# Performance work log

Measured on AMD Instinct MI355X. Metric: run time of the kernel, lower is better.

## Reference

```python
import jax, jax.numpy as jnp
import numpy as np

N, F_IN, D, R, E = 50000, 128, 96, 2, 800000


def setup_inputs() -> dict:
    key = jax.random.key(0)
    ks = jax.random.split(key, 8)
    sc = lambda k, shape: jax.random.normal(k, shape, jnp.float32) * 0.05
    return {
        "x": jax.random.normal(ks[0], (N, F_IN), jnp.float32),
        "edge_index": jax.random.randint(ks[1], (2, E), 0, N),
        "edge_attr": jax.random.uniform(ks[2], (E, R), dtype=jnp.float32),
        # nn.Linear(F_IN, D)
        "Wf": sc(ks[3], (D, F_IN)),
        "bf": jnp.zeros((D,), jnp.float32),
        # RGCNConv: per-relation weights, root weight, bias
        "W": sc(ks[4], (R, D, D)),
        "root": sc(ks[5], (D, D)),
        "bias": jnp.zeros((D,), jnp.float32),
    }


def _rgcn_conv(h, src, dst, etype, W, root, bias):
    # PyG RGCNConv (no bases/blocks, aggr='mean'):
    #   out = x @ root + bias + sum_r mean_{edges of type r}(x[src]) @ W[r]
    msg = h[src]  # [E, D] gather
    out = h @ root + bias
    for r in range(R):
        w = (etype == r).astype(h.dtype)[:, None]  # [E, 1] relation mask
        s = jax.ops.segment_sum(msg * w, dst, num_segments=N)   # [N, D] scatter-add
        cnt = jax.ops.segment_sum(w, dst, num_segments=N)       # [N, 1]
        agg = s / jnp.maximum(cnt, 1.0)                          # mean, safe for deg 0
        out = out + agg @ W[r]
    return out


def reference(x, edge_index, edge_attr, Wf, bf, W, root, bias):
    src, dst = edge_index[0], edge_index[1]
    etype = jnp.argmax(edge_attr, axis=1)  # [E]
    h = jax.nn.relu(x @ Wf.T + bf)
    for _ in range(3):
        h = jax.nn.relu(_rgcn_conv(h, src, dst, etype, W, root, bias))
    return h
```

## Files before the change

kernel.cpp:

```cpp
#include <hip/hip_runtime.h>

#define DN 96
#define FIN 128

typedef unsigned int uint_t;
typedef unsigned short ushort_t;

typedef __attribute__((ext_vector_type(8))) short short8v;
typedef __attribute__((ext_vector_type(4))) float f32x4;

#define MFMA16 __builtin_amdgcn_mfma_f32_16x16x32_bf16

struct __align__(4) U3 { uint_t x, y, z; };

__device__ __forceinline__ ushort_t f2bf(float f) {
    uint_t u = __float_as_uint(f);
    uint_t r = (u + 0x7FFFu + ((u >> 16) & 1u)) >> 16;
    return (ushort_t)r;
}
__device__ __forceinline__ float bf2f(ushort_t h) { return __uint_as_float(((uint_t)h) << 16); }
__device__ __forceinline__ float bf_lo(uint_t u) { return __uint_as_float(u << 16); }
__device__ __forceinline__ float bf_hi(uint_t u) { return __uint_as_float(u & 0xFFFF0000u); }

__device__ __forceinline__ U3 ldrow(const uint_t* __restrict__ g, int idx, int j) {
    return *(const U3*)(g + (size_t)idx * 48 + 3 * j);
}
__device__ __forceinline__ void acc6(float* s, U3 v) {
    s[0] += bf_lo(v.x); s[1] += bf_hi(v.x);
    s[2] += bf_lo(v.y); s[3] += bf_hi(v.y);
    s[4] += bf_lo(v.z); s[5] += bf_hi(v.z);
}


__global__ __launch_bounds__(256) void prep_kernel(
    const int* __restrict__ ei, const float* __restrict__ ea,
    uint_t* __restrict__ kdx, ushort_t* __restrict__ kdy,
    const float* __restrict__ root, const float* __restrict__ W, const float* __restrict__ Wf,
    ushort_t* __restrict__ Bph, ushort_t* __restrict__ Bpl,
    ushort_t* __restrict__ Wfh, ushort_t* __restrict__ Wfl,
    ushort_t* g0A, ushort_t* g1A, ushort_t* g0B, ushort_t* g1B,
    int E, int N, int KD_BLKS)
{
    int bid = blockIdx.x;
    int t = threadIdx.x;
    if (bid < KD_BLKS) {
        int e = bid * 256 + t;
        if (e < E) {
            int src = ei[e];
            int dst = ei[E + e];
            float2 a = *(const float2*)(ea + 2 * e);
            int r = (a.y > a.x) ? 1 : 0;
            kdx[e] = (uint_t)dst | ((uint_t)r << 16);
            kdy[e] = (ushort_t)src;
        }
    } else if (bid < KD_BLKS + 78) {
        if (t >= 64) return;
        int l = t;
        int fid = bid - KD_BLKS;
        if (fid < 54) {
            int ct = fid / 3, ks = fid % 3;
            int mat = ct / 6, cw = ct % 6;
            const float* M = (mat == 0) ? root : (W + (size_t)(mat - 1) * DN * DN);
            int k0 = 32 * ks + (l >> 4) * 8;
            int col = 16 * cw + (l & 15);
#pragma unroll
            for (int j = 0; j < 8; j++) {
                float v = M[(size_t)(k0 + j) * DN + col];
                ushort_t h = f2bf(v);
                size_t idx = ((size_t)fid * 64 + l) * 8 + j;
                Bph[idx] = h;
                Bpl[idx] = f2bf(v - bf2f(h));
            }
        } else {
            int f2 = fid - 54;
            int ct = f2 >> 2, ks = f2 & 3;
            int k0 = 32 * ks + (l >> 4) * 8;
            int col = 16 * ct + (l & 15);
#pragma unroll
            for (int j = 0; j < 8; j++) {
                float v = Wf[(size_t)col * FIN + k0 + j];
                ushort_t h = f2bf(v);
                size_t idx = ((size_t)f2 * 64 + l) * 8 + j;
                Wfh[idx] = h;
                Wfl[idx] = f2bf(v - bf2f(h));
            }
        }
    } else {
        int pair = bid - (KD_BLKS + 78);
        ushort_t* ga = pair ? g0B : g0A;
        ushort_t* gb = pair ? g1B : g1A;
        if (t < 96) ga[(size_t)N * DN + t] = 0;
        else if (t < 192) gb[(size_t)N * DN + (t - 96)] = 0;
    }
}


__global__ __launch_bounds__(256) void hist_part(const uint_t* __restrict__ kdx,
                                                 int* __restrict__ cnt, int E, int N, int PS) {
    int p = blockIdx.x & 7;
    int c = blockIdx.x >> 3;
    int base = c * 2048 + threadIdx.x;
#pragma unroll
    for (int i = 0; i < 8; i++) {
        int e = base + i * 256;
        if (e < E) {
            uint_t v = kdx[e];
            int dst = v & 0xFFFF;
            if (dst / PS == p) {
                int r = (v >> 16) & 1;
                atomicAdd(&cnt[r * N + dst], 1);
            }
        }
    }
}

__global__ void offsets_kernel(const int* __restrict__ cnt, int* __restrict__ total,
                               int* __restrict__ rowstart, int* __restrict__ fillptr,
                               int nbins) {
    __shared__ int sd[256];
    __shared__ int sbase;
    int t = threadIdx.x;
    int b = blockIdx.x * 256 + t;
    int v = (b < nbins) ? cnt[b] : 0;
    sd[t] = v;
    __syncthreads();
    for (int off = 1; off < 256; off <<= 1) {
        int add = (t >= off) ? sd[t - off] : 0;
        __syncthreads();
        sd[t] += add;
        __syncthreads();
    }
    if (t == 255) sbase = atomicAdd(total, sd[255]);
    __syncthreads();
    if (b < nbins) {
        int s = sbase + sd[t] - v;
        rowstart[b] = s;
        fillptr[b] = s;
    }
}


__global__ __launch_bounds__(256) void fill_part(const uint_t* __restrict__ kdx,
                            const ushort_t* __restrict__ kdy,
                            int* __restrict__ fillptr, ushort_t* __restrict__ srcs,
                            int E, int N, int PS) {
    int p = blockIdx.x & 7;
    int c = blockIdx.x >> 3;
    int base = c * 2048 + threadIdx.x;
#pragma unroll
    for (int i = 0; i < 8; i++) {
        int e = base + i * 256;
        if (e < E) {
            uint_t v = kdx[e];
            int dst = v & 0xFFFF;
            if (dst / PS == p) {
                int r = (v >> 16) & 1;
                int pos = atomicAdd(&fillptr[r * N + dst], 1);
                srcs[pos] = kdy[e];
            }
        }
    }
}


__device__ __forceinline__ void cvt8(float4 x, float4 y, short8v& hi, short8v& lo) {
    union { short8v v; ushort_t u[8]; } H, L;
    float f[8] = {x.x, x.y, x.z, x.w, y.x, y.y, y.z, y.w};
#pragma unroll
    for (int j = 0; j < 8; j++) {
        ushort_t h = f2bf(f[j]);
        H.u[j] = h;
        L.u[j] = f2bf(f[j] - bf2f(h));
    }
    hi = H.v; lo = L.v;
}


__global__ __launch_bounds__(256) void lin_gemm(
    const float* __restrict__ xin,
    const ushort_t* __restrict__ WfH, const ushort_t* __restrict__ WfL,
    const ushort_t* __restrict__ Bph, const ushort_t* __restrict__ Bpl,
    const float* __restrict__ bfv, const float* __restrict__ bias,
    float* __restrict__ hrootOut, ushort_t* __restrict__ g0Out, ushort_t* __restrict__ g1Out,
    int N)
{
    __shared__ float sout[4][16][100];
    int t = threadIdx.x;
    int l = t & 63;
    int w = t >> 6;

    int slab = blockIdx.x * 64 + w * 16;
    int row = slab + (l & 15);
    if (row >= N) row = N - 1;
    const float* xrow = xin + (size_t)row * FIN + ((l >> 4) * 8);
    short8v ah4[4], al4[4];
#pragma unroll
    for (int ks = 0; ks < 4; ks++) {
        float4 xa = *(const float4*)(xrow + 32 * ks);
        float4 xb = *(const float4*)(xrow + 32 * ks + 4);
        cvt8(xa, xb, ah4[ks], al4[ks]);
    }
#pragma unroll
    for (int ct = 0; ct < 6; ct++) {
        f32x4 hh = {0.f,0.f,0.f,0.f}, hl_ = {0.f,0.f,0.f,0.f}, lh = {0.f,0.f,0.f,0.f};
#pragma unroll
        for (int ks = 0; ks < 4; ks++) {
            size_t base = ((size_t)(ct * 4 + ks) * 64 + l) * 8;
            short8v bh = *(const short8v*)(WfH + base);
            short8v bl = *(const short8v*)(WfL + base);
            hh  = MFMA16(ah4[ks], bh, hh, 0, 0, 0);
            hl_ = MFMA16(ah4[ks], bl, hl_, 0, 0, 0);
            lh  = MFMA16(al4[ks], bh, lh, 0, 0, 0);
        }
        f32x4 acc = hh + hl_ + lh;
        int col = ct * 16 + (l & 15);
        float bv = bfv[col];
        int lr0 = (l >> 4) * 4;
#pragma unroll
        for (int r = 0; r < 4; r++) {
            float v = acc[r] + bv;
            sout[w][lr0 + r][col] = v > 0.f ? v : 0.f;
        }
    }
    __syncthreads();

    const float* srow = &sout[w][l & 15][0];
    int mbase = blockIdx.x * 64 + w * 16 + ((l >> 4) << 2);
    int k0 = (l >> 4) * 8;
    short8v ah[3], al[3];
#pragma unroll
    for (int ks = 0; ks < 3; ks++) {
        float4 xa = *(const float4*)(srow + k0 + 32 * ks);
        float4 xb = *(const float4*)(srow + k0 + 32 * ks + 4);
        cvt8(xa, xb, ah[ks], al[ks]);
    }
    for (int ct = 0; ct < 18; ct++) {
        f32x4 hh = {0.f,0.f,0.f,0.f}, hl_ = {0.f,0.f,0.f,0.f}, lh = {0.f,0.f,0.f,0.f};
#pragma unroll
        for (int ks = 0; ks < 3; ks++) {
            size_t base = ((size_t)(ct * 3 + ks) * 64 + l) * 8;
            short8v bh = *(const short8v*)(Bph + base);
            short8v bl = *(const short8v*)(Bpl + base);
            hh  = MFMA16(ah[ks], bh, hh, 0, 0, 0);
            hl_ = MFMA16(ah[ks], bl, hl_, 0, 0, 0);
            lh  = MFMA16(al[ks], bh, lh, 0, 0, 0);
        }
        f32x4 acc = hh + hl_ + lh;
        int mat = ct / 6;
        int col = (ct % 6) * 16 + (l & 15);
        if (mat == 0) {
            float bv = bias[col];
#pragma unroll
            for (int r = 0; r < 4; r++) {
                int m = mbase + r;
                if (m < N) hrootOut[(size_t)m * DN + col] = acc[r] + bv;
            }
        } else {
            ushort_t* g = (mat == 1) ? g0Out : g1Out;
#pragma unroll
            for (int r = 0; r < 4; r++) {
                int m = mbase + r;
                if (m < N) g[(size_t)m * DN + col] = f2bf(acc[r]);
            }
        }
    }
}


template <int GEMM>
__global__ __launch_bounds__(256) void layer_kernel(
    const float* __restrict__ hrootIn,
    const uint_t* __restrict__ g0In, const uint_t* __restrict__ g1In,
    const int* __restrict__ rowstart, const int* __restrict__ cnt,
    const ushort_t* __restrict__ srcs,
    const ushort_t* __restrict__ Bph, const ushort_t* __restrict__ Bpl,
    const float* __restrict__ bias,
    float* __restrict__ hrootOut, ushort_t* __restrict__ g0Out, ushort_t* __restrict__ g1Out,
    float* __restrict__ dout, int N)
{
    __shared__ float sout[16][100];
    int t = threadIdx.x;

    {
        int grp = t >> 4;
        int j = t & 15;
        int n = blockIdx.x * 16 + grp;
        bool valid = n < N;
        int nc = valid ? n : N - 1;

        const float* hr = hrootIn + (size_t)nc * DN + 6 * j;
        float2 p0 = *(const float2*)hr;
        float2 p1 = *(const float2*)(hr + 2);
        float2 p2 = *(const float2*)(hr + 4);

        float a[6] = {0.f,0.f,0.f,0.f,0.f,0.f};
#pragma unroll
        for (int r = 0; r < 2; r++) {
            int c    = valid ? cnt[r * N + nc] : 0;
            int base = valid ? rowstart[r * N + nc] : 0;
            const uint_t* g = r ? g1In : g0In;
            const ushort_t* sp = srcs + base;
            float sA[6] = {0.f,0.f,0.f,0.f,0.f,0.f};
            float sB[6] = {0.f,0.f,0.f,0.f,0.f,0.f};
            for (int e = 0; e < c; e += 8) {
                int i0 = (e + 0 < c) ? (int)sp[e + 0] : N;
                int i1 = (e + 1 < c) ? (int)sp[e + 1] : N;
                int i2 = (e + 2 < c) ? (int)sp[e + 2] : N;
                int i3 = (e + 3 < c) ? (int)sp[e + 3] : N;
                int i4 = (e + 4 < c) ? (int)sp[e + 4] : N;
                int i5 = (e + 5 < c) ? (int)sp[e + 5] : N;
                int i6 = (e + 6 < c) ? (int)sp[e + 6] : N;
                int i7 = (e + 7 < c) ? (int)sp[e + 7] : N;
                U3 v0 = ldrow(g, i0, j);
                U3 v1 = ldrow(g, i1, j);
                U3 v2 = ldrow(g, i2, j);
                U3 v3 = ldrow(g, i3, j);
                U3 v4 = ldrow(g, i4, j);
                U3 v5 = ldrow(g, i5, j);
                U3 v6 = ldrow(g, i6, j);
                U3 v7 = ldrow(g, i7, j);
                acc6(sA, v0); acc6(sB, v1); acc6(sA, v2); acc6(sB, v3);
                acc6(sA, v4); acc6(sB, v5); acc6(sA, v6); acc6(sB, v7);
            }
            float inv = (c > 0) ? 1.f / (float)c : 0.f;
#pragma unroll
            for (int k = 0; k < 6; k++) a[k] += (sA[k] + sB[k]) * inv;
        }
        float o0 = fmaxf(p0.x + a[0], 0.f);
        float o1 = fmaxf(p0.y + a[1], 0.f);
        float o2 = fmaxf(p1.x + a[2], 0.f);
        float o3 = fmaxf(p1.y + a[3], 0.f);
        float o4 = fmaxf(p2.x + a[4], 0.f);
        float o5 = fmaxf(p2.y + a[5], 0.f);
        if constexpr (GEMM) {
            float* dr = &sout[grp][6 * j];
            dr[0]=o0; dr[1]=o1; dr[2]=o2; dr[3]=o3; dr[4]=o4; dr[5]=o5;
        } else {
            if (valid) {
                float* dr = dout + (size_t)n * DN + 6 * j;
                *(float2*)(dr)     = make_float2(o0, o1);
                *(float2*)(dr + 2) = make_float2(o2, o3);
                *(float2*)(dr + 4) = make_float2(o4, o5);
            }
        }
    }

    if constexpr (!GEMM) return;
    __syncthreads();

    {
        int l = t & 63;
        int w = t >> 6;
        const float* srow = &sout[l & 15][0];
        int mbase = blockIdx.x * 16 + ((l >> 4) << 2);
        int k0 = (l >> 4) * 8;
        short8v ah[3], al[3];
#pragma unroll
        for (int ks = 0; ks < 3; ks++) {
            float4 xa = *(const float4*)(srow + k0 + 32 * ks);
            float4 xb = *(const float4*)(srow + k0 + 32 * ks + 4);
            cvt8(xa, xb, ah[ks], al[ks]);
        }
        int ctS, ctC;
        ctS = (w < 2) ? 5 * w : 10 + 4 * (w - 2);
        ctC = (w < 2) ? 5 : 4;
        for (int ci = 0; ci < ctC; ci++) {
            int ct = ctS + ci;
            f32x4 hh = {0.f,0.f,0.f,0.f}, hl_ = {0.f,0.f,0.f,0.f}, lh = {0.f,0.f,0.f,0.f};
#pragma unroll
            for (int ks = 0; ks < 3; ks++) {
                size_t base = ((size_t)(ct * 3 + ks) * 64 + l) * 8;
                short8v bh = *(const short8v*)(Bph + base);
                short8v bl = *(const short8v*)(Bpl + base);
                hh  = MFMA16(ah[ks], bh, hh, 0, 0, 0);
                hl_ = MFMA16(ah[ks], bl, hl_, 0, 0, 0);
                lh  = MFMA16(al[ks], bh, lh, 0, 0, 0);
            }
            f32x4 acc = hh + hl_ + lh;
            int mat = ct / 6;
            int col = (ct % 6) * 16 + (l & 15);
            if (mat == 0) {
                float bv = bias[col];
#pragma unroll
                for (int r = 0; r < 4; r++) {
                    int m = mbase + r;
                    if (m < N) hrootOut[(size_t)m * DN + col] = acc[r] + bv;
                }
            } else {
                ushort_t* g = (mat == 1) ? g0Out : g1Out;
#pragma unroll
                for (int r = 0; r < 4; r++) {
                    int m = mbase + r;
                    if (m < N) g[(size_t)m * DN + col] = f2bf(acc[r]);
                }
            }
        }
    }
}

extern "C" void kernel_launch(void* const* d_in, const int* in_sizes, int n_in,
                              void* d_out, int out_size, void* d_ws, size_t ws_size,
                              hipStream_t stream) {
    const float* x    = (const float*)d_in[0];
    const int*   ei   = (const int*)d_in[1];
    const float* ea   = (const float*)d_in[2];
    const float* Wf   = (const float*)d_in[3];
    const float* bf   = (const float*)d_in[4];
    const float* W    = (const float*)d_in[5];
    const float* root = (const float*)d_in[6];
    const float* bias = (const float*)d_in[7];
    float* out = (float*)d_out;

    int N = in_sizes[0] / FIN;
    int E = in_sizes[1] / 2;
    int nbins = 2 * N;
    int PS = (N + 7) / 8;
    size_t NR = (size_t)(N + 1) * DN;

    int* cnt        = (int*)d_ws;
    int* total      = cnt + nbins;
    int* rowstart   = cnt + nbins + 4;
    int* fillptr    = rowstart + nbins;
    uint_t* kdx     = (uint_t*)(fillptr + nbins);
    ushort_t* kdy   = (ushort_t*)(kdx + E);
    ushort_t* srcs  = kdy + E;
    ushort_t* Bph   = (ushort_t*)(((uintptr_t)(srcs + E) + 15) & ~(uintptr_t)15);
    ushort_t* Bpl   = Bph + 54 * 512;
    ushort_t* Wfh   = Bpl + 54 * 512;
    ushort_t* Wfl   = Wfh + 24 * 512;
    float* hrootA   = (float*)(Wfl + 24 * 512);
    ushort_t* g0A   = (ushort_t*)(hrootA + (size_t)N * DN);
    ushort_t* g1A   = g0A + NR;
    float* hrootB   = (float*)(g1A + NR);
    ushort_t* g0B   = (ushort_t*)(hrootB + (size_t)N * DN);
    ushort_t* g1B   = g0B + NR;

    hipMemsetAsync(cnt, 0, (size_t)(nbins + 1) * sizeof(int), stream);

    int KD_BLKS = (E + 255) / 256;
    int nchunk = (E + 2047) / 2048;
    int PART_BLKS = nchunk * 8;
    int blk64 = (N + 63) / 64;
    int blk16 = (N + 15) / 16;

    prep_kernel<<<KD_BLKS + 78 + 2, 256, 0, stream>>>(
        ei, ea, kdx, kdy, root, W, Wf, Bph, Bpl, Wfh, Wfl,
        g0A, g1A, g0B, g1B, E, N, KD_BLKS);
    hist_part<<<PART_BLKS, 256, 0, stream>>>(kdx, cnt, E, N, PS);
    offsets_kernel<<<(nbins + 255) / 256, 256, 0, stream>>>(cnt, total, rowstart, fillptr, nbins);
    fill_part<<<PART_BLKS, 256, 0, stream>>>(kdx, kdy, fillptr, srcs, E, N, PS);
    lin_gemm<<<blk64, 256, 0, stream>>>(
        x, Wfh, Wfl, Bph, Bpl, bf, bias, hrootA, g0A, g1A, N);
    layer_kernel<1><<<blk16, 256, 0, stream>>>(
        hrootA, (const uint_t*)g0A, (const uint_t*)g1A, rowstart, cnt, srcs,
        Bph, Bpl, bias, hrootB, g0B, g1B, nullptr, N);
    layer_kernel<1><<<blk16, 256, 0, stream>>>(
        hrootB, (const uint_t*)g0B, (const uint_t*)g1B, rowstart, cnt, srcs,
        Bph, Bpl, bias, hrootA, g0A, g1A, nullptr, N);
    layer_kernel<0><<<blk16, 256, 0, stream>>>(
        hrootA, (const uint_t*)g0A, (const uint_t*)g1A, rowstart, cnt, srcs,
        nullptr, nullptr, nullptr, nullptr, nullptr, nullptr, out, N);
}
```

Measured before the change: 294.6 us.

## Merge CSR fill and input linear GEMM into one launch with 16-row blocks

The fill_part scatter kernel and the lin_gemm input projection are combined into a single launch. The first blocks do the CSR fill and the remaining blocks run the GEMM, so the two independent jobs can overlap and one launch is removed. The GEMM part is reworked from 64-row blocks (each wave doing a 16-row slab) to 16-row blocks, with the four waves sharing column tiles. This raises block count and lowers shared memory per block, but it reloads the weight fragments more often per row.

```diff
diff --git a/kernel.cpp b/kernel.cpp
--- a/kernel.cpp
+++ b/kernel.cpp
@@ -140,29 +140,6 @@
 }
 
 
-__global__ __launch_bounds__(256) void fill_part(const uint_t* __restrict__ kdx,
-                            const ushort_t* __restrict__ kdy,
-                            int* __restrict__ fillptr, ushort_t* __restrict__ srcs,
-                            int E, int N, int PS) {
-    int p = blockIdx.x & 7;
-    int c = blockIdx.x >> 3;
-    int base = c * 2048 + threadIdx.x;
-#pragma unroll
-    for (int i = 0; i < 8; i++) {
-        int e = base + i * 256;
-        if (e < E) {
-            uint_t v = kdx[e];
-            int dst = v & 0xFFFF;
-            if (dst / PS == p) {
-                int r = (v >> 16) & 1;
-                int pos = atomicAdd(&fillptr[r * N + dst], 1);
-                srcs[pos] = kdy[e];
-            }
-        }
-    }
-}
-
-
 __device__ __forceinline__ void cvt8(float4 x, float4 y, short8v& hi, short8v& lo) {
     union { short8v v; ushort_t u[8]; } H, L;
     float f[8] = {x.x, x.y, x.z, x.w, y.x, y.y, y.z, y.w};
@@ -176,91 +153,123 @@
 }
 
 
-__global__ __launch_bounds__(256) void lin_gemm(
+__global__ __launch_bounds__(256) void fill_lin(
+    const uint_t* __restrict__ kdx, const ushort_t* __restrict__ kdy,
+    int* __restrict__ fillptr, ushort_t* __restrict__ srcs,
     const float* __restrict__ xin,
     const ushort_t* __restrict__ WfH, const ushort_t* __restrict__ WfL,
     const ushort_t* __restrict__ Bph, const ushort_t* __restrict__ Bpl,
     const float* __restrict__ bfv, const float* __restrict__ bias,
     float* __restrict__ hrootOut, ushort_t* __restrict__ g0Out, ushort_t* __restrict__ g1Out,
-    int N)
+    int E, int N, int PS, int FILL_BLKS)
 {
-    __shared__ float sout[4][16][100];
+    __shared__ float sout[16][100];
     int t = threadIdx.x;
+
+    if (blockIdx.x < FILL_BLKS) {
+        int p = blockIdx.x & 7;
+        int c = blockIdx.x >> 3;
+        int base = c * 2048 + t;
+#pragma unroll
+        for (int i = 0; i < 8; i++) {
+            int e = base + i * 256;
+            if (e < E) {
+                uint_t v = kdx[e];
+                int dst = v & 0xFFFF;
+                if (dst / PS == p) {
+                    int r = (v >> 16) & 1;
+                    int pos = atomicAdd(&fillptr[r * N + dst], 1);
+                    srcs[pos] = kdy[e];
+                }
+            }
+        }
+        return;
+    }
+
+    int bid2 = blockIdx.x - FILL_BLKS;
     int l = t & 63;
     int w = t >> 6;
 
-    int slab = blockIdx.x * 64 + w * 16;
-    int row = slab + (l & 15);
-    if (row >= N) row = N - 1;
-    const float* xrow = xin + (size_t)row * FIN + ((l >> 4) * 8);
-    short8v ah4[4], al4[4];
-#pragma unroll
-    for (int ks = 0; ks < 4; ks++) {
-        float4 xa = *(const float4*)(xrow + 32 * ks);
-        float4 xb = *(const float4*)(xrow + 32 * ks + 4);
-        cvt8(xa, xb, ah4[ks], al4[ks]);
-    }
-#pragma unroll
-    for (int ct = 0; ct < 6; ct++) {
-        f32x4 hh = {0.f,0.f,0.f,0.f}, hl_ = {0.f,0.f,0.f,0.f}, lh = {0.f,0.f,0.f,0.f};
+    {
+        int slab = bid2 * 16;
+        int row = slab + (l & 15);
+        if (row >= N) row = N - 1;
+        const float* xrow = xin + (size_t)row * FIN + ((l >> 4) * 8);
+        short8v ah4[4], al4[4];
 #pragma unroll
         for (int ks = 0; ks < 4; ks++) {
-            size_t base = ((size_t)(ct * 4 + ks) * 64 + l) * 8;
-            short8v bh = *(const short8v*)(WfH + base);
-            short8v bl = *(const short8v*)(WfL + base);
-            hh  = MFMA16(ah4[ks], bh, hh, 0, 0, 0);
-            hl_ = MFMA16(ah4[ks], bl, hl_, 0, 0, 0);
-            lh  = MFMA16(al4[ks], bh, lh, 0, 0, 0);
-        }
-        f32x4 acc = hh + hl_ + lh;
-        int col = ct * 16 + (l & 15);
-        float bv = bfv[col];
-        int lr0 = (l >> 4) * 4;
-#pragma unroll
-        for (int r = 0; r < 4; r++) {
-            float v = acc[r] + bv;
-            sout[w][lr0 + r][col] = v > 0.f ? v : 0.f;
+            float4 xa = *(const float4*)(xrow + 32 * ks);
+            float4 xb = *(const float4*)(xrow + 32 * ks + 4);
+            cvt8(xa, xb, ah4[ks], al4[ks]);
+        }
+        int nct = (w < 2) ? 2 : 1;
+        for (int ci = 0; ci < nct; ci++) {
+            int ct = w + ci * 4;
+            f32x4 hh = {0.f,0.f,0.f,0.f}, hl_ = {0.f,0.f,0.f,0.f}, lh = {0.f,0.f,0.f,0.f};
+#pragma unroll
+            for (int ks = 0; ks < 4; ks++) {
+                size_t base = ((size_t)(ct * 4 + ks) * 64 + l) * 8;
+                short8v bh = *(const short8v*)(WfH + base);
+                short8v bl = *(const short8v*)(WfL + base);
+                hh  = MFMA16(ah4[ks], bh, hh, 0, 0, 0);
+                hl_ = MFMA16(ah4[ks], bl, hl_, 0, 0, 0);
+                lh  = MFMA16(al4[ks], bh, lh, 0, 0, 0);
+            }
+            f32x4 acc = hh + hl_ + lh;
+            int col = ct * 16 + (l & 15);
+            float bv = bfv[col];
+            int lr0 = (l >> 4) * 4;
+#pragma unroll
+            for (int r = 0; r < 4; r++) {
+                float v = acc[r] + bv;
+                sout[lr0 + r][col] = v > 0.f ? v : 0.f;
+            }
         }
     }
     __syncthreads();
 
-    const float* srow = &sout[w][l & 15][0];
-    int mbase = blockIdx.x * 64 + w * 16 + ((l >> 4) << 2);
-    int k0 = (l >> 4) * 8;
-    short8v ah[3], al[3];
-#pragma unroll
-    for (int ks = 0; ks < 3; ks++) {
-        float4 xa = *(const float4*)(srow + k0 + 32 * ks);
-        float4 xb = *(const float4*)(srow + k0 + 32 * ks + 4);
-        cvt8(xa, xb, ah[ks], al[ks]);
-    }
-    for (int ct = 0; ct < 18; ct++) {
-        f32x4 hh = {0.f,0.f,0.f,0.f}, hl_ = {0.f,0.f,0.f,0.f}, lh = {0.f,0.f,0.f,0.f};
+    {
+        const float* srow = &sout[l & 15][0];
+        int mbase = bid2 * 16 + ((l >> 4) << 2);
+        int k0 = (l >> 4) * 8;
+        short8v ah[3], al[3];
 #pragma unroll
         for (int ks = 0; ks < 3; ks++) {
-            size_t base = ((size_t)(ct * 3 + ks) * 64 + l) * 8;
-            short8v bh = *(const short8v*)(Bph + base);
-            short8v bl = *(const short8v*)(Bpl + base);
-            hh  = MFMA16(ah[ks], bh, hh, 0, 0, 0);
-            hl_ = MFMA16(ah[ks], bl, hl_, 0, 0, 0);
-            lh  = MFMA16(al[ks], bh, lh, 0, 0, 0);
-        }
-        f32x4 acc = hh + hl_ + lh;
-        int mat = ct / 6;
-        int col = (ct % 6) * 16 + (l & 15);
-        if (mat == 0) {
-            float bv = bias[col];
-#pragma unroll
-            for (int r = 0; r < 4; r++) {
-                int m = mbase + r;
-                if (m < N) hrootOut[(size_t)m * DN + col] = acc[r] + bv;
-            }
-        } else {
-            ushort_t* g = (mat == 1) ? g0Out : g1Out;
-#pragma unroll
-            for (int r = 0; r < 4; r++) {
-                int m = mbase + r;
-                if (m < N) g[(size_t)m * DN + col] = f2bf(acc[r]);
+            float4 xa = *(const float4*)(srow + k0 + 32 * ks);
+            float4 xb = *(const float4*)(srow + k0 + 32 * ks + 4);
+            cvt8(xa, xb, ah[ks], al[ks]);
+        }
+        int ctS = (w < 2) ? 5 * w : 10 + 4 * (w - 2);
+        int ctC = (w < 2) ? 5 : 4;
+        for (int ci = 0; ci < ctC; ci++) {
+            int ct = ctS + ci;
+            f32x4 hh = {0.f,0.f,0.f,0.f}, hl_ = {0.f,0.f,0.f,0.f}, lh = {0.f,0.f,0.f,0.f};
+#pragma unroll
+            for (int ks = 0; ks < 3; ks++) {
+                size_t base = ((size_t)(ct * 3 + ks) * 64 + l) * 8;
+                short8v bh = *(const short8v*)(Bph + base);
+                short8v bl = *(const short8v*)(Bpl + base);
+                hh  = MFMA16(ah[ks], bh, hh, 0, 0, 0);
+                hl_ = MFMA16(ah[ks], bl, hl_, 0, 0, 0);
+                lh  = MFMA16(al[ks], bh, lh, 0, 0, 0);
+            }
+            f32x4 acc = hh + hl_ + lh;
+            int mat = ct / 6;
+            int col = (ct % 6) * 16 + (l & 15);
+            if (mat == 0) {
+                float bv = bias[col];
+#pragma unroll
+                for (int r = 0; r < 4; r++) {
+                    int m = mbase + r;
+                    if (m < N) hrootOut[(size_t)m * DN + col] = acc[r] + bv;
+                }
+            } else {
+                ushort_t* g = (mat == 1) ? g0Out : g1Out;
+#pragma unroll
+                for (int r = 0; r < 4; r++) {
+                    int m = mbase + r;
+                    if (m < N) g[(size_t)m * DN + col] = f2bf(acc[r]);
+                }
             }
         }
     }
@@ -361,9 +370,8 @@
             float4 xb = *(const float4*)(srow + k0 + 32 * ks + 4);
             cvt8(xa, xb, ah[ks], al[ks]);
         }
-        int ctS, ctC;
-        ctS = (w < 2) ? 5 * w : 10 + 4 * (w - 2);
-        ctC = (w < 2) ? 5 : 4;
+        int ctS = (w < 2) ? 5 * w : 10 + 4 * (w - 2);
+        int ctC = (w < 2) ? 5 : 4;
         for (int ci = 0; ci < ctC; ci++) {
             int ct = ctS + ci;
             f32x4 hh = {0.f,0.f,0.f,0.f}, hl_ = {0.f,0.f,0.f,0.f}, lh = {0.f,0.f,0.f,0.f};
@@ -440,7 +448,6 @@
     int KD_BLKS = (E + 255) / 256;
     int nchunk = (E + 2047) / 2048;
     int PART_BLKS = nchunk * 8;
-    int blk64 = (N + 63) / 64;
     int blk16 = (N + 15) / 16;
 
     prep_kernel<<<KD_BLKS + 78 + 2, 256, 0, stream>>>(
@@ -448,9 +455,9 @@
         g0A, g1A, g0B, g1B, E, N, KD_BLKS);
     hist_part<<<PART_BLKS, 256, 0, stream>>>(kdx, cnt, E, N, PS);
     offsets_kernel<<<(nbins + 255) / 256, 256, 0, stream>>>(cnt, total, rowstart, fillptr, nbins);
-    fill_part<<<PART_BLKS, 256, 0, stream>>>(kdx, kdy, fillptr, srcs, E, N, PS);
-    lin_gemm<<<blk64, 256, 0, stream>>>(
-        x, Wfh, Wfl, Bph, Bpl, bf, bias, hrootA, g0A, g1A, N);
+    fill_lin<<<PART_BLKS + blk16, 256, 0, stream>>>(
+        kdx, kdy, fillptr, srcs, x, Wfh, Wfl, Bph, Bpl, bf, bias,
+        hrootA, g0A, g1A, E, N, PS, PART_BLKS);
     layer_kernel<1><<<blk16, 256, 0, stream>>>(
         hrootA, (const uint_t*)g0A, (const uint_t*)g1A, rowstart, cnt, srcs,
         Bph, Bpl, bias, hrootB, g0B, g1B, nullptr, N);
```

Result: faster. 287.3 us (-2.5%).
